# Kernel tuning notes

Hardware: AMD Instinct MI355X
Metric: run time of the kernel (lower is better)

Reference implementation:

```python
import jax, jax.numpy as jnp
import numpy as np

NUM_POINTS = 200000
IN_FEATURES = 128
OUT_FEATURES = 128
NUM_RELATIONS = 128
NUM_BLOCKS = 16
IN_BLOCK = IN_FEATURES // NUM_BLOCKS   # 8
OUT_BLOCK = OUT_FEATURES // NUM_BLOCKS  # 8


def setup_inputs() -> dict:
    key = jax.random.key(0)
    k1, k2, k3 = jax.random.split(key, 3)
    x = jax.random.normal(k1, (NUM_POINTS, IN_FEATURES), dtype=jnp.float32)
    # glorot-uniform init of the per-relation block-diagonal weights
    blocks = jax.nn.initializers.glorot_uniform()(
        k2, (NUM_RELATIONS, NUM_BLOCKS, IN_BLOCK, OUT_BLOCK), jnp.float32)
    rel = jax.random.randint(k3, (NUM_POINTS,), 0, NUM_RELATIONS)
    return {"x": x, "blocks": blocks, "rel": rel}


def reference(x, blocks, rel):
    # x: [p, num_blocks*in_block]; blocks: [R, nb, ib, ob]; rel: [p] int
    p = x.shape[0]
    R, nb, ib, ob = blocks.shape
    x_by_block = x.reshape(p, nb, ib)                 # [p, nb, ib]
    relation_blocks = blocks[rel]                     # gather: [p, nb, ib, ob]
    transformed = jnp.einsum('pnio,pni->pno', relation_blocks, x_by_block)
    return transformed.reshape(p, nb * ob)            # [p, out_features]
```

## Files before the change

### kernel.cpp

```cpp
#include <hip/hip_runtime.h>


typedef float v4f __attribute__((ext_vector_type(4)));

__device__ __forceinline__ float4 dpp_swap1(float4 v) {
    union { float4 f; int i[4]; } a, b;
    a.f = v;
    b.i[0] = __builtin_amdgcn_update_dpp(0, a.i[0], 0xB1, 0xF, 0xF, true);
    b.i[1] = __builtin_amdgcn_update_dpp(0, a.i[1], 0xB1, 0xF, 0xF, true);
    b.i[2] = __builtin_amdgcn_update_dpp(0, a.i[2], 0xB1, 0xF, 0xF, true);
    b.i[3] = __builtin_amdgcn_update_dpp(0, a.i[3], 0xB1, 0xF, 0xF, true);
    return b.f;
}

__global__ __launch_bounds__(1024) void k_fused(
    const float* __restrict__ x, const float* __restrict__ w,
    const int* __restrict__ rel, float* __restrict__ out, int npoints)
{
    __shared__ float4 wlds[128][64];

    const int q = blockIdx.x >> 6;
    const int b = blockIdx.x & 63;

    const float4* wsrc = reinterpret_cast<const float4*>(w);
    #pragma unroll
    for (int t = 0; t < 8; ++t) {
        int f   = threadIdx.x + t * 1024;
        int r   = f >> 6;
        int lo  = f & 63;
        int nls = lo >> 4;
        int k   = f & 15;
        wlds[r][((k << 2) | nls) ^ (r & 63)] = wsrc[r * 256 + q * 64 + lo];
    }
    __syncthreads();

    const int lane = threadIdx.x & 63;
    const int wv   = threadIdx.x >> 6;
    const int pt8  = lane >> 3;
    const int j    = lane & 7;
    const int nl   = j >> 1;
    const int h    = j & 1;

    const int chunk = (npoints + 63) >> 6;
    const int plo   = b * chunk;
    const int phi   = min(plo + chunk, npoints);
    const int phim1 = phi - 1;

    int gB = plo + wv * 32;
    if (gB >= phi) return;

    const float4* xv = reinterpret_cast<const float4*>(x) + q * 8 + j;
    float4*       ov = reinterpret_cast<float4*>(out) + q * 8 + j;

    auto comp = [&](int r1, float4 xa, int p1) {
        float4 xo  = dpp_swap1(xa);
        float4 xlo = h ? xo  : xa;
        float4 xhi = h ? xa : xo;
        const int s   = r1 & 63;
        const int thi = s & 0x38;
        const int t0  = ((h << 2) | nl) ^ (s & 7);
        const float4* base = wlds[r1];
        float xf[8] = {xlo.x, xlo.y, xlo.z, xlo.w,
                       xhi.x, xhi.y, xhi.z, xhi.w};
        float a0 = 0.f, a1 = 0.f, a2 = 0.f, a3 = 0.f;
        #pragma unroll
        for (int i = 0; i < 8; ++i) {
            float4 wv4 = base[((i << 3) ^ thi) | t0];
            float xi = xf[i];
            a0 = fmaf(xi, wv4.x, a0);
            a1 = fmaf(xi, wv4.y, a1);
            a2 = fmaf(xi, wv4.z, a2);
            a3 = fmaf(xi, wv4.w, a3);
        }
        if (p1 < phi) {
            v4f val = {a0, a1, a2, a3};
            __builtin_nontemporal_store(val,
                reinterpret_cast<v4f*>(&ov[(size_t)p1 * 32]));
        }
    };

    int    rr0, rr1, rr2, rr3;
    float4 xr0, xr1, xr2, xr3;
    {
        int p0 = min(gB +  0 + pt8, phim1);
        int p1 = min(gB +  8 + pt8, phim1);
        int p2 = min(gB + 16 + pt8, phim1);
        int p3 = min(gB + 24 + pt8, phim1);
        rr0 = rel[p0]; rr1 = rel[p1]; rr2 = rel[p2]; rr3 = rel[p3];
        xr0 = xv[(size_t)p0 * 32]; xr1 = xv[(size_t)p1 * 32];
        xr2 = xv[(size_t)p2 * 32]; xr3 = xv[(size_t)p3 * 32];
    }

    while (true) {
        int gN = gB + 512;
        int    rn0, rn1, rn2, rn3;
        float4 xn0, xn1, xn2, xn3;
        if (gN < phi) {
            int p0 = min(gN +  0 + pt8, phim1);
            int p1 = min(gN +  8 + pt8, phim1);
            int p2 = min(gN + 16 + pt8, phim1);
            int p3 = min(gN + 24 + pt8, phim1);
            xn0 = xv[(size_t)p0 * 32]; xn1 = xv[(size_t)p1 * 32];
            xn2 = xv[(size_t)p2 * 32]; xn3 = xv[(size_t)p3 * 32];
            rn0 = rel[p0]; rn1 = rel[p1]; rn2 = rel[p2]; rn3 = rel[p3];
        }

        comp(rr0, xr0, gB +  0 + pt8);
        comp(rr1, xr1, gB +  8 + pt8);
        comp(rr2, xr2, gB + 16 + pt8);
        comp(rr3, xr3, gB + 24 + pt8);

        if (gN >= phi) break;
        gB = gN;
        rr0 = rn0; rr1 = rn1; rr2 = rn2; rr3 = rn3;
        xr0 = xn0; xr1 = xn1; xr2 = xn2; xr3 = xn3;
    }
}

__global__ __launch_bounds__(256) void brl_kernel(
    const float* __restrict__ x, const float* __restrict__ w,
    const int* __restrict__ rel, float* __restrict__ out, int npoints)
{
    int tid = blockIdx.x * 256 + threadIdx.x;
    int p = tid >> 4;
    if (p >= npoints) return;
    int n = tid & 15;
    int r = rel[p];
    const float4* xv = reinterpret_cast<const float4*>(x + (size_t)p * 128 + n * 8);
    float4 x0 = xv[0], x1 = xv[1];
    float xf[8] = {x0.x, x0.y, x0.z, x0.w, x1.x, x1.y, x1.z, x1.w};
    const float4* wv = reinterpret_cast<const float4*>(w + ((size_t)r * 16 + n) * 64);
    float acc[8] = {0.f, 0.f, 0.f, 0.f, 0.f, 0.f, 0.f, 0.f};
    #pragma unroll
    for (int i = 0; i < 8; ++i) {
        float4 w0 = wv[2 * i], w1 = wv[2 * i + 1];
        float wf[8] = {w0.x, w0.y, w0.z, w0.w, w1.x, w1.y, w1.z, w1.w};
        #pragma unroll
        for (int o = 0; o < 8; ++o) acc[o] = fmaf(xf[i], wf[o], acc[o]);
    }
    float4* ov = reinterpret_cast<float4*>(out + (size_t)p * 128 + n * 8);
    ov[0] = make_float4(acc[0], acc[1], acc[2], acc[3]);
    ov[1] = make_float4(acc[4], acc[5], acc[6], acc[7]);
}

extern "C" void kernel_launch(void* const* d_in, const int* in_sizes, int n_in,
                              void* d_out, int out_size, void* d_ws, size_t ws_size,
                              hipStream_t stream) {
    const float* x   = (const float*)d_in[0];
    const float* w   = (const float*)d_in[1];
    const int*   rel = (const int*)d_in[2];
    float*       out = (float*)d_out;

    int npoints = in_sizes[2];
    int R = in_sizes[1] / 1024;

    if (R == 128 && in_sizes[0] == npoints * 128) {
        k_fused<<<256, 1024, 0, stream>>>(x, w, rel, out, npoints);
    } else {
        int total = npoints * 16;
        brl_kernel<<<(total + 255) / 256, 256, 0, stream>>>(x, w, rel, out, npoints);
    }
}
```

Before: 195.7 us.

## Replace batched prefetch with rolling four-deep per-point load pipeline

Each wave now handles 8 points per step with a stride of 128 points instead of processing 32 consecutive points per iteration. It keeps a four-stage rolling register queue of x and rel loads and issues one new load per computed point, keeping loads in flight continuously rather than in batches. The nontemporal output store is replaced by a plain float4 store. This trades per-iteration loop overhead and a different, more interleaved access pattern across waves for smoother memory-latency hiding.

```diff
diff --git a/kernel.cpp b/kernel.cpp
--- a/kernel.cpp
+++ b/kernel.cpp
@@ -1,7 +1,5 @@
 #include <hip/hip_runtime.h>
 
-
-typedef float v4f __attribute__((ext_vector_type(4)));
 
 __device__ __forceinline__ float4 dpp_swap1(float4 v) {
     union { float4 f; int i[4]; } a, b;
@@ -46,15 +44,17 @@
     const int phi   = min(plo + chunk, npoints);
     const int phim1 = phi - 1;
 
-    int gB = plo + wv * 32;
-    if (gB >= phi) return;
+    int g = plo + wv * 8;
+    if (g >= phi) return;
 
     const float4* xv = reinterpret_cast<const float4*>(x) + q * 8 + j;
     float4*       ov = reinterpret_cast<float4*>(out) + q * 8 + j;
 
+    const int STEP = 128;
+
     auto comp = [&](int r1, float4 xa, int p1) {
         float4 xo  = dpp_swap1(xa);
-        float4 xlo = h ? xo  : xa;
+        float4 xlo = h ? xo : xa;
         float4 xhi = h ? xa : xo;
         const int s   = r1 & 63;
         const int thi = s & 0x38;
@@ -66,54 +66,44 @@
         #pragma unroll
         for (int i = 0; i < 8; ++i) {
             float4 wv4 = base[((i << 3) ^ thi) | t0];
-            float xi = xf[i];
-            a0 = fmaf(xi, wv4.x, a0);
-            a1 = fmaf(xi, wv4.y, a1);
-            a2 = fmaf(xi, wv4.z, a2);
-            a3 = fmaf(xi, wv4.w, a3);
+            float xi = wv4.x, dummy;
+            (void)dummy;
+            float xi1 = xf[i];
+            a0 = fmaf(xi1, wv4.x, a0);
+            a1 = fmaf(xi1, wv4.y, a1);
+            a2 = fmaf(xi1, wv4.z, a2);
+            a3 = fmaf(xi1, wv4.w, a3);
+            (void)xi;
         }
-        if (p1 < phi) {
-            v4f val = {a0, a1, a2, a3};
-            __builtin_nontemporal_store(val,
-                reinterpret_cast<v4f*>(&ov[(size_t)p1 * 32]));
-        }
+        if (p1 < phi)
+            ov[(size_t)p1 * 32] = make_float4(a0, a1, a2, a3);
     };
 
-    int    rr0, rr1, rr2, rr3;
-    float4 xr0, xr1, xr2, xr3;
+    int    r0, r1s, r2s, r3s;
+    float4 x0, x1s, x2s, x3s;
     {
-        int p0 = min(gB +  0 + pt8, phim1);
-        int p1 = min(gB +  8 + pt8, phim1);
-        int p2 = min(gB + 16 + pt8, phim1);
-        int p3 = min(gB + 24 + pt8, phim1);
-        rr0 = rel[p0]; rr1 = rel[p1]; rr2 = rel[p2]; rr3 = rel[p3];
-        xr0 = xv[(size_t)p0 * 32]; xr1 = xv[(size_t)p1 * 32];
-        xr2 = xv[(size_t)p2 * 32]; xr3 = xv[(size_t)p3 * 32];
+        int p0 = min(g +   0 + pt8, phim1);
+        int p1 = min(g + 128 + pt8, phim1);
+        int p2 = min(g + 256 + pt8, phim1);
+        int p3 = min(g + 384 + pt8, phim1);
+        x0  = xv[(size_t)p0 * 32]; x1s = xv[(size_t)p1 * 32];
+        x2s = xv[(size_t)p2 * 32]; x3s = xv[(size_t)p3 * 32];
+        r0  = rel[p0]; r1s = rel[p1]; r2s = rel[p2]; r3s = rel[p3];
     }
 
     while (true) {
-        int gN = gB + 512;
-        int    rn0, rn1, rn2, rn3;
-        float4 xn0, xn1, xn2, xn3;
-        if (gN < phi) {
-            int p0 = min(gN +  0 + pt8, phim1);
-            int p1 = min(gN +  8 + pt8, phim1);
-            int p2 = min(gN + 16 + pt8, phim1);
-            int p3 = min(gN + 24 + pt8, phim1);
-            xn0 = xv[(size_t)p0 * 32]; xn1 = xv[(size_t)p1 * 32];
-            xn2 = xv[(size_t)p2 * 32]; xn3 = xv[(size_t)p3 * 32];
-            rn0 = rel[p0]; rn1 = rel[p1]; rn2 = rel[p2]; rn3 = rel[p3];
-        }
+        int pc = min(g + 4 * STEP + pt8, phim1);
+        float4 xn = xv[(size_t)pc * 32];
+        int    rn = rel[pc];
 
-        comp(rr0, xr0, gB +  0 + pt8);
-        comp(rr1, xr1, gB +  8 + pt8);
-        comp(rr2, xr2, gB + 16 + pt8);
-        comp(rr3, xr3, gB + 24 + pt8);
+        comp(r0, x0, g + pt8);
 
-        if (gN >= phi) break;
-        gB = gN;
-        rr0 = rn0; rr1 = rn1; rr2 = rn2; rr3 = rn3;
-        xr0 = xn0; xr1 = xn1; xr2 = xn2; xr3 = xn3;
+        if (g + STEP >= phi) break;
+        g += STEP;
+        r0  = r1s; x0  = x1s;
+        r1s = r2s; x1s = x2s;
+        r2s = r3s; x2s = x3s;
+        r3s = rn;  x3s = xn;
     }
 }
 
```

Result: faster. 190.6 us (-2.6%).
